# Optimization experiments

Measured on AMD Instinct MI355X. Metric: run time of the kernel, lower is better.

## Reference

```python
import jax, jax.numpy as jnp
import numpy as np

N = 50000      # total nodes
E = 400000     # edges (before self-loops)
F_IN = 75      # atom features
H = 4          # GAT heads (layers 1,2)
C = 128        # hidden_channels
G = 512        # graphs in batch
EPS_BN = 1e-5


def setup_inputs() -> dict:
    key = jax.random.key(0)
    ks = jax.random.split(key, 32)
    inp = {}
    inp["x"] = jax.random.normal(ks[0], (N, F_IN), jnp.float32)
    inp["edge_index"] = jax.random.randint(ks[1], (2, E), 0, N, dtype=jnp.int32)
    inp["batch"] = jnp.sort(jax.random.randint(ks[2], (N,), 0, G, dtype=jnp.int32))
    # (in_dim, heads, out_per_head, concat)
    dims = [(F_IN, H, C, True), (H * C, H, C, True), (H * C, 1, C, False)]
    i = 3
    for li, (din, h, c, concat) in enumerate(dims, 1):
        dout = h * c if concat else c
        s = 1.0 / np.sqrt(din)
        inp[f"W{li}"] = jax.random.normal(ks[i], (din, h * c), jnp.float32) * s
        inp[f"as{li}"] = jax.random.normal(ks[i + 1], (h, c), jnp.float32) * 0.1
        inp[f"ad{li}"] = jax.random.normal(ks[i + 2], (h, c), jnp.float32) * 0.1
        inp[f"b{li}"] = jnp.zeros((dout,), jnp.float32)
        inp[f"g{li}"] = jnp.ones((dout,), jnp.float32)
        inp[f"bt{li}"] = jnp.zeros((dout,), jnp.float32)
        inp[f"rm{li}"] = jax.random.normal(ks[i + 3], (dout,), jnp.float32) * 0.05
        inp[f"rv{li}"] = jnp.ones((dout,), jnp.float32)
        i += 4
    return inp


def gat_layer(x, src, dst, W, a_src, a_dst, b, heads, c_out, concat):
    # x: [N, Fin] -> h: [N, H, C]
    n = x.shape[0]
    h = (x @ W).reshape(n, heads, c_out)
    # per-node attention logits [N, H]
    al_s = jnp.sum(h * a_src[None], axis=-1)
    al_d = jnp.sum(h * a_dst[None], axis=-1)
    # per-edge logits + leaky relu (PyG GATConv, slope 0.2)
    e = jax.nn.leaky_relu(al_s[src] + al_d[dst], negative_slope=0.2)  # [E, H]
    # segment softmax over destination nodes
    emax = jax.ops.segment_max(e, dst, num_segments=n)
    p = jnp.exp(e - emax[dst])
    denom = jax.ops.segment_sum(p, dst, num_segments=n)
    alpha = p / (denom[dst] + 1e-16)
    # weighted message aggregation
    msg = h[src] * alpha[:, :, None]            # [E, H, C]
    out = jax.ops.segment_sum(msg, dst, num_segments=n)  # [N, H, C]
    out = out.reshape(n, heads * c_out) if concat else out.mean(axis=1)
    return out + b


def bn_eval(x, g, bt, rm, rv):
    return (x - rm) * g * jax.lax.rsqrt(rv + EPS_BN) + bt


def reference(x, edge_index, batch,
              W1, as1, ad1, b1, g1, bt1, rm1, rv1,
              W2, as2, ad2, b2, g2, bt2, rm2, rv2,
              W3, as3, ad3, b3, g3, bt3, rm3, rv3):
    n = x.shape[0]
    ar = jnp.arange(n, dtype=edge_index.dtype)
    # GATConv adds self-loops by default
    src = jnp.concatenate([edge_index[0], ar])
    dst = jnp.concatenate([edge_index[1], ar])

    h = gat_layer(x, src, dst, W1, as1, ad1, b1, H, C, True)
    h = jax.nn.relu(bn_eval(h, g1, bt1, rm1, rv1))   # dropout off (eval)
    h = gat_layer(h, src, dst, W2, as2, ad2, b2, H, C, True)
    h = jax.nn.relu(bn_eval(h, g2, bt2, rm2, rv2))
    h = gat_layer(h, src, dst, W3, as3, ad3, b3, 1, C, False)
    h = bn_eval(h, g3, bt3, rm3, rv3)

    # global mean + max pool over graphs
    ones = jnp.ones((n,), h.dtype)
    cnt = jnp.maximum(jax.ops.segment_sum(ones, batch, num_segments=G), 1.0)
    gmean = jax.ops.segment_sum(h, batch, num_segments=G) / cnt[:, None]
    gmax = jax.ops.segment_max(h, batch, num_segments=G)
    gmax = jnp.where(jnp.isfinite(gmax), gmax, 0.0)  # guard empty graphs
    return jnp.concatenate([gmean, gmax], axis=1)    # [G, 2*C]
```

## Files before the change

### kernel.cpp

```cpp
#include <hip/hip_runtime.h>

typedef unsigned short u16;
typedef unsigned int u32;
typedef __attribute__((ext_vector_type(8))) short s16x8;
typedef __attribute__((ext_vector_type(4))) float f32x4;

__device__ __forceinline__ float bf2f(u32 u) {
    return __uint_as_float(u << 16);
}
__device__ __forceinline__ u16 f2bf(float f) {
    u32 x = __float_as_uint(f);
    u32 r = (x + 0x7fffu + ((x >> 16) & 1u)) >> 16;
    return (u16)r;
}

__device__ __forceinline__ void gload16(const u16* g, u16* l) {
    __builtin_amdgcn_global_load_lds(
        (const __attribute__((address_space(1))) unsigned int*)g,
        (__attribute__((address_space(3))) unsigned int*)l,
        16, 0, 0);
}

__device__ __forceinline__ float lk60(float e) {
    e = (e > 0.f) ? e : 0.2f * e;
    return fminf(e, 60.f);
}

__global__ __launch_bounds__(256) void cvt_all_k(
    const float* __restrict__ x, const float* __restrict__ W1,
    const float* __restrict__ W2, const float* __restrict__ W3,
    u16* __restrict__ xb, u16* __restrict__ Wt1,
    u16* __restrict__ Wt2, u16* __restrict__ Wt3, int N, int Mp)
{
    const int i = blockIdx.x * 256 + threadIdx.x;
    const int n1 = Mp * 96;
    const int n2 = 512 * 96;
    const int n3 = 512 * 512;
    const int n4 = 128 * 512;
    if (i < n1) {
        const int r = i / 96, c = i - r * 96;
        xb[i] = f2bf((r < N && c < 75) ? x[(size_t)r * 75 + c] : 0.f);
    } else if (i < n1 + n2) {
        const int j = i - n1;
        const int n = j / 96, k = j - n * 96;
        Wt1[j] = f2bf(k < 75 ? W1[(size_t)k * 512 + n] : 0.f);
    } else if (i < n1 + n2 + n3) {
        const int j = i - n1 - n2;
        const int n = j >> 9, k = j & 511;
        Wt2[j] = f2bf(W2[(size_t)k * 512 + n]);
    } else if (i < n1 + n2 + n3 + n4) {
        const int j = i - n1 - n2 - n3;
        const int n = j >> 9, k = j & 511;
        Wt3[j] = f2bf(W3[(size_t)k * 128 + n]);
    }
}

__global__ __launch_bounds__(256) void mgemm_k(
    const u16* __restrict__ A, const u16* __restrict__ Bt, u16* __restrict__ C,
    const float* __restrict__ avs, const float* __restrict__ avd,
    float* __restrict__ als, float* __restrict__ ald,
    int M, int K, int Ncol, int H, int NXB)
{
    __shared__ u16 Al[2][128 * 32];
    __shared__ u16 Bl[2][128 * 32];
    const int t = threadIdx.x;
    const int lane = t & 63;
    const int wid = t >> 6;
    const int wr = wid >> 1, wc = wid & 1;
    const int rr = lane & 15, q = lane >> 4;

    const int dd = blockIdx.x;
    const int xcd = dd & 7, ii = dd >> 3;
    const int gpx = (int)(gridDim.x >> 3) / NXB;
    const int yb = xcd * gpx + ((NXB == 4) ? (ii >> 2) : ii);
    const int head = (NXB == 4) ? (ii & 3) : 0;
    const int m0 = yb * 128, n0 = head * 128;

    f32x4 acc[4][4];
#pragma unroll
    for (int m = 0; m < 4; ++m)
#pragma unroll
        for (int n = 0; n < 4; ++n) acc[m][n] = (f32x4){0.f, 0.f, 0.f, 0.f};

    auto stage = [&](int b, int k0) {
#pragma unroll
        for (int i2 = 0; i2 < 2; ++i2) {
            const int si = i2 * 256 + t;
            const int r = si >> 2, s = si & 3;
            const int g = s ^ ((r >> 1) & 3);
            gload16(A  + (size_t)(m0 + r) * K + k0 + g * 8, &Al[b][si * 8]);
            gload16(Bt + (size_t)(n0 + r) * K + k0 + g * 8, &Bl[b][si * 8]);
        }
    };

    const int nk = K >> 5;
    stage(0, 0);
    __syncthreads();
    int buf = 0;
    for (int kt = 0; kt < nk; ++kt) {
        if (kt + 1 < nk) stage(buf ^ 1, (kt + 1) << 5);
        s16x8 af[4], bfr[4];
#pragma unroll
        for (int m = 0; m < 4; ++m) {
            const int r = wr * 64 + m * 16 + rr;
            af[m] = *reinterpret_cast<const s16x8*>(&Al[buf][r * 32 + ((q ^ ((r >> 1) & 3)) << 3)]);
        }
#pragma unroll
        for (int n = 0; n < 4; ++n) {
            const int r = wc * 64 + n * 16 + rr;
            bfr[n] = *reinterpret_cast<const s16x8*>(&Bl[buf][r * 32 + ((q ^ ((r >> 1) & 3)) << 3)]);
        }
#pragma unroll
        for (int m = 0; m < 4; ++m)
#pragma unroll
            for (int n = 0; n < 4; ++n)
                acc[m][n] = __builtin_amdgcn_mfma_f32_16x16x32_bf16(af[m], bfr[n], acc[m][n], 0, 0, 0);
        __syncthreads();
        buf ^= 1;
    }

#pragma unroll
    for (int m = 0; m < 4; ++m) {
        const int row_b = m0 + wr * 64 + m * 16 + q * 4;
#pragma unroll
        for (int j = 0; j < 4; ++j) {
            const int row = row_b + j;
            if (row < M) {
#pragma unroll
                for (int n = 0; n < 4; ++n) {
                    const int col = n0 + wc * 64 + n * 16 + rr;
                    C[(size_t)row * Ncol + col] = f2bf(acc[m][n][j]);
                }
            }
        }
    }

    float asv[4], adv[4];
#pragma unroll
    for (int n = 0; n < 4; ++n) {
        const int c = wc * 64 + n * 16 + rr;
        asv[n] = avs[head * 128 + c];
        adv[n] = avd[head * 128 + c];
    }
    float* lps = (float*)&Al[0][0];
    float* lpd = lps + 256;
#pragma unroll
    for (int m = 0; m < 4; ++m)
#pragma unroll
        for (int j = 0; j < 4; ++j) {
            float ps = 0.f, pd = 0.f;
#pragma unroll
            for (int n = 0; n < 4; ++n) {
                ps += acc[m][n][j] * asv[n];
                pd += acc[m][n][j] * adv[n];
            }
#pragma unroll
            for (int off = 1; off < 16; off <<= 1) {
                ps += __shfl_xor(ps, off, 64);
                pd += __shfl_xor(pd, off, 64);
            }
            if (rr == 0) {
                const int r = wr * 64 + m * 16 + q * 4 + j;
                lps[wc * 128 + r] = ps;
                lpd[wc * 128 + r] = pd;
            }
        }
    __syncthreads();
    if (t < 128) {
        const int row = m0 + t;
        if (row < M) {
            als[(size_t)row * H + head] = lps[t] + lps[128 + t];
            ald[(size_t)row * H + head] = lpd[t] + lpd[128 + t];
        }
    }
}

__global__ void count_k(const int* __restrict__ edst, int* __restrict__ cnt, int E_, int N_)
{
    const int i = blockIdx.x * 256 + threadIdx.x;
    if (i >= E_ + N_) return;
    const int d = (i < E_) ? edst[i] : (i - E_);
    atomicAdd(&cnt[d], 1);
}

#define SCAN_B 256
__global__ void scan1_k(const int* __restrict__ cnt, int* __restrict__ part,
                        int* __restrict__ bsum, int n)
{
    __shared__ int sm[SCAN_B];
    const int idx = blockIdx.x * SCAN_B + threadIdx.x;
    int v = (idx < n) ? cnt[idx] : 0;
    sm[threadIdx.x] = v;
    __syncthreads();
    for (int off = 1; off < SCAN_B; off <<= 1) {
        int t2 = (threadIdx.x >= off) ? sm[threadIdx.x - off] : 0;
        __syncthreads();
        sm[threadIdx.x] += t2;
        __syncthreads();
    }
    if (idx < n) part[idx] = sm[threadIdx.x];
    if (threadIdx.x == SCAN_B - 1) bsum[blockIdx.x] = sm[threadIdx.x];
}

__global__ void scan2_k(int* __restrict__ bsum, int nb)
{
    __shared__ int sm[SCAN_B];
    const int t = threadIdx.x;
    int v = (t < nb) ? bsum[t] : 0;
    sm[t] = v;
    __syncthreads();
    for (int off = 1; off < SCAN_B; off <<= 1) {
        int t2 = (t >= off) ? sm[t - off] : 0;
        __syncthreads();
        sm[t] += t2;
        __syncthreads();
    }
    if (t < nb) bsum[t] = sm[t] - v;
}

__global__ void scan3_k(const int* __restrict__ part, const int* __restrict__ boff,
                        int* __restrict__ offs, int n)
{
    const int idx = blockIdx.x * SCAN_B + threadIdx.x;
    if (idx < n) offs[idx + 1] = part[idx] + boff[idx / SCAN_B];
    if (idx == 0) offs[0] = 0;
}

__global__ void scatter_k(const int* __restrict__ esrc, const int* __restrict__ edst,
                          const int* __restrict__ offs, int* __restrict__ fill,
                          int* __restrict__ csr, int E_, int N_)
{
    const int i = blockIdx.x * 256 + threadIdx.x;
    if (i >= E_ + N_) return;
    int s, d;
    if (i < E_) { s = esrc[i]; d = edst[i]; } else { s = d = i - E_; }
    const int pos = offs[d] + atomicAdd(&fill[d], 1);
    csr[pos] = s;
}

template<bool RELU>
__global__ __launch_bounds__(256) void agg512_k(
    const u16* __restrict__ hsrc, const int* __restrict__ offs,
    const int* __restrict__ csr, const float* __restrict__ als,
    const float* __restrict__ ald, const float* __restrict__ bias,
    const float* __restrict__ gam, const float* __restrict__ bet,
    const float* __restrict__ rmean, const float* __restrict__ rvar,
    u16* __restrict__ outp, int N)
{
    const int lane = threadIdx.x & 63;
    const int dst = blockIdx.x * 4 + (threadIdx.x >> 6);
    if (dst >= N) return;
    const int ch0 = lane * 8;
    const int hd = lane >> 4;

    const float advh = ald[(size_t)dst * 4 + hd];
    const int rs = offs[dst], re = offs[dst + 1];

    float acc[8] = {};
    float smw = 0.f;
    int s = rs;
    for (; s + 4 <= re; s += 4) {
        int sn[4];
#pragma unroll
        for (int u = 0; u < 4; ++u) sn[u] = csr[s + u];
        int4 r[4];
#pragma unroll
        for (int u = 0; u < 4; ++u)
            r[u] = *reinterpret_cast<const int4*>(hsrc + (size_t)sn[u] * 512 + ch0);
        float aa[4];
#pragma unroll
        for (int u = 0; u < 4; ++u)
            aa[u] = __expf(lk60(als[(size_t)sn[u] * 4 + hd] + advh));
#pragma unroll
        for (int u = 0; u < 4; ++u) {
            smw += aa[u];
            const u32 rr2[4] = {(u32)r[u].x, (u32)r[u].y, (u32)r[u].z, (u32)r[u].w};
#pragma unroll
            for (int qq = 0; qq < 4; ++qq) {
                acc[2*qq]   += aa[u] * bf2f(rr2[qq] & 0xffffu);
                acc[2*qq+1] += aa[u] * bf2f(rr2[qq] >> 16);
            }
        }
    }
    for (; s < re; ++s) {
        const int sn = csr[s];
        const float a = __expf(lk60(als[(size_t)sn * 4 + hd] + advh));
        smw += a;
        const int4 r = *reinterpret_cast<const int4*>(hsrc + (size_t)sn * 512 + ch0);
        const u32 rr2[4] = {(u32)r.x, (u32)r.y, (u32)r.z, (u32)r.w};
#pragma unroll
        for (int qq = 0; qq < 4; ++qq) {
            acc[2*qq]   += a * bf2f(rr2[qq] & 0xffffu);
            acc[2*qq+1] += a * bf2f(rr2[qq] >> 16);
        }
    }
    const float inv = 1.f / (smw + 1e-16f);

    u16 ob[8];
#pragma unroll
    for (int j = 0; j < 8; ++j) {
        const int ch = ch0 + j;
        const float scale = gam[ch] * rsqrtf(rvar[ch] + 1e-5f);
        float val = (acc[j] * inv + bias[ch] - rmean[ch]) * scale + bet[ch];
        if (RELU) val = fmaxf(val, 0.f);
        ob[j] = f2bf(val);
    }
    int4 w;
    w.x = (int)((u32)ob[0] | ((u32)ob[1] << 16));
    w.y = (int)((u32)ob[2] | ((u32)ob[3] << 16));
    w.z = (int)((u32)ob[4] | ((u32)ob[5] << 16));
    w.w = (int)((u32)ob[6] | ((u32)ob[7] << 16));
    *reinterpret_cast<int4*>(outp + (size_t)dst * 512 + ch0) = w;
}

__global__ __launch_bounds__(256) void agg128_k(
    const u16* __restrict__ hsrc, const int* __restrict__ offs,
    const int* __restrict__ csr, const float* __restrict__ als,
    const float* __restrict__ ald, const float* __restrict__ bias,
    const float* __restrict__ gam, const float* __restrict__ bet,
    const float* __restrict__ rmean, const float* __restrict__ rvar,
    u16* __restrict__ outp, int N)
{
    const int tid = threadIdx.x;
    const int w = tid >> 6, g = (tid >> 4) & 3, l = tid & 15;
    const int dst = blockIdx.x * 16 + w * 4 + g;
    if (dst >= N) return;
    const int ch0 = l * 8;

    const float advh = ald[dst];
    const int rs = offs[dst], re = offs[dst + 1];

    float acc[8] = {};
    float smw = 0.f;
    int s = rs;
    for (; s + 4 <= re; s += 4) {
        int sn[4];
#pragma unroll
        for (int u = 0; u < 4; ++u) sn[u] = csr[s + u];
        int4 r[4];
#pragma unroll
        for (int u = 0; u < 4; ++u)
            r[u] = *reinterpret_cast<const int4*>(hsrc + (size_t)sn[u] * 128 + ch0);
        float aa[4];
#pragma unroll
        for (int u = 0; u < 4; ++u)
            aa[u] = __expf(lk60(als[sn[u]] + advh));
#pragma unroll
        for (int u = 0; u < 4; ++u) {
            smw += aa[u];
            const u32 rr2[4] = {(u32)r[u].x, (u32)r[u].y, (u32)r[u].z, (u32)r[u].w};
#pragma unroll
            for (int qq = 0; qq < 4; ++qq) {
                acc[2*qq]   += aa[u] * bf2f(rr2[qq] & 0xffffu);
                acc[2*qq+1] += aa[u] * bf2f(rr2[qq] >> 16);
            }
        }
    }
    for (; s < re; ++s) {
        const int sn = csr[s];
        const float a = __expf(lk60(als[sn] + advh));
        smw += a;
        const int4 r = *reinterpret_cast<const int4*>(hsrc + (size_t)sn * 128 + ch0);
        const u32 rr2[4] = {(u32)r.x, (u32)r.y, (u32)r.z, (u32)r.w};
#pragma unroll
        for (int qq = 0; qq < 4; ++qq) {
            acc[2*qq]   += a * bf2f(rr2[qq] & 0xffffu);
            acc[2*qq+1] += a * bf2f(rr2[qq] >> 16);
        }
    }
    const float inv = 1.f / (smw + 1e-16f);

    u16 ob[8];
#pragma unroll
    for (int j = 0; j < 8; ++j) {
        const int ch = ch0 + j;
        const float scale = gam[ch] * rsqrtf(rvar[ch] + 1e-5f);
        float val = (acc[j] * inv + bias[ch] - rmean[ch]) * scale + bet[ch];
        ob[j] = f2bf(val);
    }
    int4 wv;
    wv.x = (int)((u32)ob[0] | ((u32)ob[1] << 16));
    wv.y = (int)((u32)ob[2] | ((u32)ob[3] << 16));
    wv.z = (int)((u32)ob[4] | ((u32)ob[5] << 16));
    wv.w = (int)((u32)ob[6] | ((u32)ob[7] << 16));
    *reinterpret_cast<int4*>(outp + (size_t)dst * 128 + ch0) = wv;
}

__global__ __launch_bounds__(128) void pool_k(
    const u16* __restrict__ h3, const int* __restrict__ batch,
    float* __restrict__ out, int N)
{
    const int g = blockIdx.x;
    const int t = threadIdx.x;
    int lo = 0, hi = N;
    while (lo < hi) { int mid = (lo + hi) >> 1; if (batch[mid] < g) lo = mid + 1; else hi = mid; }
    const int s0 = lo;
    lo = 0; hi = N;
    while (lo < hi) { int mid = (lo + hi) >> 1; if (batch[mid] < g + 1) lo = mid + 1; else hi = mid; }
    const int s1 = lo;
    float sum = 0.f, mx = -1e30f;
    for (int n = s0; n < s1; ++n) {
        const float v = bf2f((u32)h3[(size_t)n * 128 + t]);
        sum += v;
        mx = fmaxf(mx, v);
    }
    const int cnt = s1 - s0;
    out[(size_t)g * 256 + t]       = cnt ? sum / (float)cnt : 0.f;
    out[(size_t)g * 256 + 128 + t] = cnt ? mx : 0.f;
}

extern "C" void kernel_launch(void* const* d_in, const int* in_sizes, int n_in,
                              void* d_out, int out_size, void* d_ws, size_t ws_size,
                              hipStream_t stream)
{
    const float* x   = (const float*)d_in[0];
    const int* ei    = (const int*)d_in[1];
    const int* batch = (const int*)d_in[2];
    const float* W1  = (const float*)d_in[3];
    const float* as1 = (const float*)d_in[4];
    const float* ad1 = (const float*)d_in[5];
    const float* b1  = (const float*)d_in[6];
    const float* g1  = (const float*)d_in[7];
    const float* bt1 = (const float*)d_in[8];
    const float* rm1 = (const float*)d_in[9];
    const float* rv1 = (const float*)d_in[10];
    const float* W2  = (const float*)d_in[11];
    const float* as2 = (const float*)d_in[12];
    const float* ad2 = (const float*)d_in[13];
    const float* b2  = (const float*)d_in[14];
    const float* g2  = (const float*)d_in[15];
    const float* bt2 = (const float*)d_in[16];
    const float* rm2 = (const float*)d_in[17];
    const float* rv2 = (const float*)d_in[18];
    const float* W3  = (const float*)d_in[19];
    const float* as3 = (const float*)d_in[20];
    const float* ad3 = (const float*)d_in[21];
    const float* b3  = (const float*)d_in[22];
    const float* g3  = (const float*)d_in[23];
    const float* bt3 = (const float*)d_in[24];
    const float* rm3 = (const float*)d_in[25];
    const float* rv3 = (const float*)d_in[26];

    const int Nn = in_sizes[2];
    const int Ee = in_sizes[1] / 2;
    const int ET = Ee + Nn;
    const int Gg = out_size / 256;
    const int Mp = 392 * 128;

    char* ws = (char*)d_ws;
    size_t o = 0;
    auto alc = [&](size_t bytes) { size_t r = o; o = (o + bytes + 255) & ~(size_t)255; return r; };
    u16*  hA   = (u16*)(ws + alc((size_t)Mp * 512 * 2));
    u16*  hB   = (u16*)(ws + alc((size_t)Mp * 512 * 2));
    u16*  xb   = (u16*)(ws + alc((size_t)Mp * 96 * 2));
    u16*  Wt1  = (u16*)(ws + alc((size_t)512 * 96 * 2));
    u16*  Wt2  = (u16*)(ws + alc((size_t)512 * 512 * 2));
    u16*  Wt3  = (u16*)(ws + alc((size_t)128 * 512 * 2));
    float* als = (float*)(ws + alc((size_t)Nn * 4 * 4));
    float* ald = (float*)(ws + alc((size_t)Nn * 4 * 4));
    int*  cnt  = (int*)(ws + alc((size_t)2 * Nn * 4));
    int*  fill = cnt + Nn;
    int*  offs = (int*)(ws + alc((size_t)(Nn + 1) * 4));
    int*  part = (int*)(ws + alc((size_t)Nn * 4));
    int*  bsum = (int*)(ws + alc((size_t)SCAN_B * 4));
    int*  csr  = (int*)(ws + alc((size_t)ET * 4));
    (void)ws_size; (void)n_in;

    hipMemsetAsync(cnt, 0, (size_t)2 * Nn * 4, stream);
    const int ETB = (ET + 255) / 256;
    count_k<<<ETB, 256, 0, stream>>>(ei + Ee, cnt, Ee, Nn);
    const int nb = (Nn + SCAN_B - 1) / SCAN_B;
    scan1_k<<<nb, SCAN_B, 0, stream>>>(cnt, part, bsum, Nn);
    scan2_k<<<1, SCAN_B, 0, stream>>>(bsum, nb);
    scan3_k<<<nb, SCAN_B, 0, stream>>>(part, bsum, offs, Nn);
    scatter_k<<<ETB, 256, 0, stream>>>(ei, ei + Ee, offs, fill, csr, Ee, Nn);

    {
        const int tot = Mp * 96 + 512 * 96 + 512 * 512 + 128 * 512;
        cvt_all_k<<<(tot + 255) / 256, 256, 0, stream>>>(x, W1, W2, W3,
                                                         xb, Wt1, Wt2, Wt3, Nn, Mp);
    }

    const int nwb4  = (Nn + 3) / 4;
    const int nwb16 = (Nn + 15) / 16;
    const int nwg4 = 392 * 4;
    const int nwg1 = 392;

    mgemm_k<<<nwg4, 256, 0, stream>>>(xb, Wt1, hA, as1, ad1, als, ald, Nn, 96, 512, 4, 4);
    agg512_k<true><<<nwb4, 256, 0, stream>>>(hA, offs, csr, als, ald,
                                             b1, g1, bt1, rm1, rv1, hB, Nn);
    mgemm_k<<<nwg4, 256, 0, stream>>>(hB, Wt2, hA, as2, ad2, als, ald, Nn, 512, 512, 4, 4);
    agg512_k<true><<<nwb4, 256, 0, stream>>>(hA, offs, csr, als, ald,
                                             b2, g2, bt2, rm2, rv2, hB, Nn);
    mgemm_k<<<nwg1, 256, 0, stream>>>(hB, Wt3, hA, as3, ad3, als, ald, Nn, 512, 128, 1, 1);
    agg128_k<<<nwb16, 256, 0, stream>>>(hA, offs, csr, als, ald,
                                        b3, g3, bt3, rm3, rv3, hB, Nn);
    pool_k<<<Gg, 128, 0, stream>>>(hB, batch, (float*)d_out, Nn);
}
```

Measured before the change: 370.7 us.

## Split 512-wide aggregation into channel slices and merge prep/scan kernels

The 512-channel aggregation kernel now assigns each block one 64-channel slice (of eight) across 32 destinations, with 8 lanes per destination, instead of one wavefront per destination covering all channels. This gives more, smaller gathers and makes blocks with the same slice index share a head's feature columns, aiming at better cache locality and load balance. Separately, the degree count is fused into the conversion kernel and the three-kernel scan is replaced by a single 1024-thread block scan, cutting launch overhead. In exchange, the csr index list and attention logits are re-read once per slice, and the single-block scan is serial per thread.

```diff
diff --git a/kernel.cpp b/kernel.cpp
--- a/kernel.cpp
+++ b/kernel.cpp
@@ -26,13 +26,21 @@
     return fminf(e, 60.f);
 }
 
-__global__ __launch_bounds__(256) void cvt_all_k(
+__global__ __launch_bounds__(256) void prep_k(
+    const int* __restrict__ edst,  int* __restrict__ cnt, int E_,
     const float* __restrict__ x, const float* __restrict__ W1,
     const float* __restrict__ W2, const float* __restrict__ W3,
     u16* __restrict__ xb, u16* __restrict__ Wt1,
-    u16* __restrict__ Wt2, u16* __restrict__ Wt3, int N, int Mp)
-{
-    const int i = blockIdx.x * 256 + threadIdx.x;
+    u16* __restrict__ Wt2, u16* __restrict__ Wt3, int N, int Mp, int ETB)
+{
+    if ((int)blockIdx.x < ETB) {
+        const int i = blockIdx.x * 256 + threadIdx.x;
+        if (i >= E_ + N) return;
+        const int d = (i < E_) ? edst[i] : (i - E_);
+        atomicAdd(&cnt[d], 1);
+        return;
+    }
+    const int i = ((int)blockIdx.x - ETB) * 256 + threadIdx.x;
     const int n1 = Mp * 96;
     const int n2 = 512 * 96;
     const int n3 = 512 * 512;
@@ -55,6 +63,34 @@
     }
 }
 
+__global__ __launch_bounds__(1024) void scan_one_k(
+    const int* __restrict__ cnt, int* __restrict__ offs, int n)
+{
+    __shared__ int part[1024];
+    const int t = threadIdx.x;
+    const int per = (n + 1023) / 1024;
+    const int base = t * per;
+    int sum = 0;
+    for (int i = 0; i < per; ++i) {
+        const int idx = base + i;
+        if (idx < n) { sum += cnt[idx]; offs[idx + 1] = sum; }
+    }
+    part[t] = sum;
+    __syncthreads();
+    for (int off = 1; off < 1024; off <<= 1) {
+        int v = (t >= off) ? part[t - off] : 0;
+        __syncthreads();
+        part[t] += v;
+        __syncthreads();
+    }
+    const int excl = part[t] - sum;
+    for (int i = 0; i < per; ++i) {
+        const int idx = base + i;
+        if (idx < n) offs[idx + 1] += excl;
+    }
+    if (t == 0) offs[0] = 0;
+}
+
 __global__ __launch_bounds__(256) void mgemm_k(
     const u16* __restrict__ A, const u16* __restrict__ Bt, u16* __restrict__ C,
     const float* __restrict__ avs, const float* __restrict__ avd,
@@ -175,57 +211,6 @@
     }
 }
 
-__global__ void count_k(const int* __restrict__ edst, int* __restrict__ cnt, int E_, int N_)
-{
-    const int i = blockIdx.x * 256 + threadIdx.x;
-    if (i >= E_ + N_) return;
-    const int d = (i < E_) ? edst[i] : (i - E_);
-    atomicAdd(&cnt[d], 1);
-}
-
-#define SCAN_B 256
-__global__ void scan1_k(const int* __restrict__ cnt, int* __restrict__ part,
-                        int* __restrict__ bsum, int n)
-{
-    __shared__ int sm[SCAN_B];
-    const int idx = blockIdx.x * SCAN_B + threadIdx.x;
-    int v = (idx < n) ? cnt[idx] : 0;
-    sm[threadIdx.x] = v;
-    __syncthreads();
-    for (int off = 1; off < SCAN_B; off <<= 1) {
-        int t2 = (threadIdx.x >= off) ? sm[threadIdx.x - off] : 0;
-        __syncthreads();
-        sm[threadIdx.x] += t2;
-        __syncthreads();
-    }
-    if (idx < n) part[idx] = sm[threadIdx.x];
-    if (threadIdx.x == SCAN_B - 1) bsum[blockIdx.x] = sm[threadIdx.x];
-}
-
-__global__ void scan2_k(int* __restrict__ bsum, int nb)
-{
-    __shared__ int sm[SCAN_B];
-    const int t = threadIdx.x;
-    int v = (t < nb) ? bsum[t] : 0;
-    sm[t] = v;
-    __syncthreads();
-    for (int off = 1; off < SCAN_B; off <<= 1) {
-        int t2 = (t >= off) ? sm[t - off] : 0;
-        __syncthreads();
-        sm[t] += t2;
-        __syncthreads();
-    }
-    if (t < nb) bsum[t] = sm[t] - v;
-}
-
-__global__ void scan3_k(const int* __restrict__ part, const int* __restrict__ boff,
-                        int* __restrict__ offs, int n)
-{
-    const int idx = blockIdx.x * SCAN_B + threadIdx.x;
-    if (idx < n) offs[idx + 1] = part[idx] + boff[idx / SCAN_B];
-    if (idx == 0) offs[0] = 0;
-}
-
 __global__ void scatter_k(const int* __restrict__ esrc, const int* __restrict__ edst,
                           const int* __restrict__ offs, int* __restrict__ fill,
                           int* __restrict__ csr, int E_, int N_)
@@ -239,7 +224,7 @@
 }
 
 template<bool RELU>
-__global__ __launch_bounds__(256) void agg512_k(
+__global__ __launch_bounds__(256) void agg512s_k(
     const u16* __restrict__ hsrc, const int* __restrict__ offs,
     const int* __restrict__ csr, const float* __restrict__ als,
     const float* __restrict__ ald, const float* __restrict__ bias,
@@ -247,11 +232,16 @@
     const float* __restrict__ rmean, const float* __restrict__ rvar,
     u16* __restrict__ outp, int N)
 {
-    const int lane = threadIdx.x & 63;
-    const int dst = blockIdx.x * 4 + (threadIdx.x >> 6);
+    const int blk = blockIdx.x;
+    const int slice = blk & 7, gi = blk >> 3;
+    const int t = threadIdx.x;
+    const int w = t >> 6;
+    const int lane = t & 63;
+    const int g = lane >> 3, l = lane & 7;
+    const int dst = gi * 32 + w * 8 + g;
     if (dst >= N) return;
-    const int ch0 = lane * 8;
-    const int hd = lane >> 4;
+    const int ch0 = slice * 64 + l * 8;
+    const int hd = slice >> 1;
 
     const float advh = ald[(size_t)dst * 4 + hd];
     const int rs = offs[dst], re = offs[dst + 1];
@@ -305,12 +295,12 @@
         if (RELU) val = fmaxf(val, 0.f);
         ob[j] = f2bf(val);
     }
-    int4 w;
-    w.x = (int)((u32)ob[0] | ((u32)ob[1] << 16));
-    w.y = (int)((u32)ob[2] | ((u32)ob[3] << 16));
-    w.z = (int)((u32)ob[4] | ((u32)ob[5] << 16));
-    w.w = (int)((u32)ob[6] | ((u32)ob[7] << 16));
-    *reinterpret_cast<int4*>(outp + (size_t)dst * 512 + ch0) = w;
+    int4 wv;
+    wv.x = (int)((u32)ob[0] | ((u32)ob[1] << 16));
+    wv.y = (int)((u32)ob[2] | ((u32)ob[3] << 16));
+    wv.z = (int)((u32)ob[4] | ((u32)ob[5] << 16));
+    wv.w = (int)((u32)ob[6] | ((u32)ob[7] << 16));
+    *reinterpret_cast<int4*>(outp + (size_t)dst * 512 + ch0) = wv;
 }
 
 __global__ __launch_bounds__(256) void agg128_k(
@@ -461,37 +451,33 @@
     int*  cnt  = (int*)(ws + alc((size_t)2 * Nn * 4));
     int*  fill = cnt + Nn;
     int*  offs = (int*)(ws + alc((size_t)(Nn + 1) * 4));
-    int*  part = (int*)(ws + alc((size_t)Nn * 4));
-    int*  bsum = (int*)(ws + alc((size_t)SCAN_B * 4));
     int*  csr  = (int*)(ws + alc((size_t)ET * 4));
     (void)ws_size; (void)n_in;
 
+    const int ETB = (ET + 255) / 256;
+
     hipMemsetAsync(cnt, 0, (size_t)2 * Nn * 4, stream);
-    const int ETB = (ET + 255) / 256;
-    count_k<<<ETB, 256, 0, stream>>>(ei + Ee, cnt, Ee, Nn);
-    const int nb = (Nn + SCAN_B - 1) / SCAN_B;
-    scan1_k<<<nb, SCAN_B, 0, stream>>>(cnt, part, bsum, Nn);
-    scan2_k<<<1, SCAN_B, 0, stream>>>(bsum, nb);
-    scan3_k<<<nb, SCAN_B, 0, stream>>>(part, bsum, offs, Nn);
+    {
+        const int cvt_tot = Mp * 96 + 512 * 96 + 512 * 512 + 128 * 512;
+        const int cvtB = (cvt_tot + 255) / 256;
+        prep_k<<<ETB + cvtB, 256, 0, stream>>>(ei + Ee, cnt, Ee,
+                                               x, W1, W2, W3,
+                                               xb, Wt1, Wt2, Wt3, Nn, Mp, ETB);
+    }
+    scan_one_k<<<1, 1024, 0, stream>>>(cnt, offs, Nn);
     scatter_k<<<ETB, 256, 0, stream>>>(ei, ei + Ee, offs, fill, csr, Ee, Nn);
 
-    {
-        const int tot = Mp * 96 + 512 * 96 + 512 * 512 + 128 * 512;
-        cvt_all_k<<<(tot + 255) / 256, 256, 0, stream>>>(x, W1, W2, W3,
-                                                         xb, Wt1, Wt2, Wt3, Nn, Mp);
-    }
-
-    const int nwb4  = (Nn + 3) / 4;
+    const int nbs32 = (Nn + 31) / 32;
     const int nwb16 = (Nn + 15) / 16;
     const int nwg4 = 392 * 4;
     const int nwg1 = 392;
 
     mgemm_k<<<nwg4, 256, 0, stream>>>(xb, Wt1, hA, as1, ad1, als, ald, Nn, 96, 512, 4, 4);
-    agg512_k<true><<<nwb4, 256, 0, stream>>>(hA, offs, csr, als, ald,
-                                             b1, g1, bt1, rm1, rv1, hB, Nn);
+    agg512s_k<true><<<8 * nbs32, 256, 0, stream>>>(hA, offs, csr, als, ald,
+                                                   b1, g1, bt1, rm1, rv1, hB, Nn);
     mgemm_k<<<nwg4, 256, 0, stream>>>(hB, Wt2, hA, as2, ad2, als, ald, Nn, 512, 512, 4, 4);
-    agg512_k<true><<<nwb4, 256, 0, stream>>>(hA, offs, csr, als, ald,
-                                             b2, g2, bt2, rm2, rv2, hB, Nn);
+    agg512s_k<true><<<8 * nbs32, 256, 0, stream>>>(hA, offs, csr, als, ald,
+                                                   b2, g2, bt2, rm2, rv2, hB, Nn);
     mgemm_k<<<nwg1, 256, 0, stream>>>(hB, Wt3, hA, as3, ad3, als, ald, Nn, 512, 128, 1, 1);
     agg128_k<<<nwb16, 256, 0, stream>>>(hA, offs, csr, als, ald,
                                         b3, g3, bt3, rm3, rv3, hB, Nn);
```

New measurement: 509.1 us. 1.37x slower.

## Slice 512-channel aggregation across blocks by channel group and fuse count with conversion

Applied to the files above, without the earlier changes.

The 512-channel GAT aggregation kernel is remapped so that each block handles one 64-channel slice for 32 destination nodes, with 8 lanes per node, instead of one wavefront covering all 512 channels of a node. The slice index sits in the low bits of the block id, so neighbouring blocks touch the same rows of the source features, which is meant to improve cache locality on the gathers and balance irregular degrees. The in-degree counting kernel is also merged into the weight/input conversion kernel to save a launch. In exchange, CSR offsets, attention logits and edge indices are reread once per slice, eight times in total.

```diff
diff --git a/kernel.cpp b/kernel.cpp
--- a/kernel.cpp
+++ b/kernel.cpp
@@ -26,13 +26,21 @@
     return fminf(e, 60.f);
 }
 
-__global__ __launch_bounds__(256) void cvt_all_k(
+__global__ __launch_bounds__(256) void prep_k(
+    const int* __restrict__ edst,  int* __restrict__ cnt, int E_,
     const float* __restrict__ x, const float* __restrict__ W1,
     const float* __restrict__ W2, const float* __restrict__ W3,
     u16* __restrict__ xb, u16* __restrict__ Wt1,
-    u16* __restrict__ Wt2, u16* __restrict__ Wt3, int N, int Mp)
-{
-    const int i = blockIdx.x * 256 + threadIdx.x;
+    u16* __restrict__ Wt2, u16* __restrict__ Wt3, int N, int Mp, int ETB)
+{
+    if ((int)blockIdx.x < ETB) {
+        const int i = blockIdx.x * 256 + threadIdx.x;
+        if (i >= E_ + N) return;
+        const int d = (i < E_) ? edst[i] : (i - E_);
+        atomicAdd(&cnt[d], 1);
+        return;
+    }
+    const int i = ((int)blockIdx.x - ETB) * 256 + threadIdx.x;
     const int n1 = Mp * 96;
     const int n2 = 512 * 96;
     const int n3 = 512 * 512;
@@ -55,134 +63,6 @@
     }
 }
 
-__global__ __launch_bounds__(256) void mgemm_k(
-    const u16* __restrict__ A, const u16* __restrict__ Bt, u16* __restrict__ C,
-    const float* __restrict__ avs, const float* __restrict__ avd,
-    float* __restrict__ als, float* __restrict__ ald,
-    int M, int K, int Ncol, int H, int NXB)
-{
-    __shared__ u16 Al[2][128 * 32];
-    __shared__ u16 Bl[2][128 * 32];
-    const int t = threadIdx.x;
-    const int lane = t & 63;
-    const int wid = t >> 6;
-    const int wr = wid >> 1, wc = wid & 1;
-    const int rr = lane & 15, q = lane >> 4;
-
-    const int dd = blockIdx.x;
-    const int xcd = dd & 7, ii = dd >> 3;
-    const int gpx = (int)(gridDim.x >> 3) / NXB;
-    const int yb = xcd * gpx + ((NXB == 4) ? (ii >> 2) : ii);
-    const int head = (NXB == 4) ? (ii & 3) : 0;
-    const int m0 = yb * 128, n0 = head * 128;
-
-    f32x4 acc[4][4];
-#pragma unroll
-    for (int m = 0; m < 4; ++m)
-#pragma unroll
-        for (int n = 0; n < 4; ++n) acc[m][n] = (f32x4){0.f, 0.f, 0.f, 0.f};
-
-    auto stage = [&](int b, int k0) {
-#pragma unroll
-        for (int i2 = 0; i2 < 2; ++i2) {
-            const int si = i2 * 256 + t;
-            const int r = si >> 2, s = si & 3;
-            const int g = s ^ ((r >> 1) & 3);
-            gload16(A  + (size_t)(m0 + r) * K + k0 + g * 8, &Al[b][si * 8]);
-            gload16(Bt + (size_t)(n0 + r) * K + k0 + g * 8, &Bl[b][si * 8]);
-        }
-    };
-
-    const int nk = K >> 5;
-    stage(0, 0);
-    __syncthreads();
-    int buf = 0;
-    for (int kt = 0; kt < nk; ++kt) {
-        if (kt + 1 < nk) stage(buf ^ 1, (kt + 1) << 5);
-        s16x8 af[4], bfr[4];
-#pragma unroll
-        for (int m = 0; m < 4; ++m) {
-            const int r = wr * 64 + m * 16 + rr;
-            af[m] = *reinterpret_cast<const s16x8*>(&Al[buf][r * 32 + ((q ^ ((r >> 1) & 3)) << 3)]);
-        }
-#pragma unroll
-        for (int n = 0; n < 4; ++n) {
-            const int r = wc * 64 + n * 16 + rr;
-            bfr[n] = *reinterpret_cast<const s16x8*>(&Bl[buf][r * 32 + ((q ^ ((r >> 1) & 3)) << 3)]);
-        }
-#pragma unroll
-        for (int m = 0; m < 4; ++m)
-#pragma unroll
-            for (int n = 0; n < 4; ++n)
-                acc[m][n] = __builtin_amdgcn_mfma_f32_16x16x32_bf16(af[m], bfr[n], acc[m][n], 0, 0, 0);
-        __syncthreads();
-        buf ^= 1;
-    }
-
-#pragma unroll
-    for (int m = 0; m < 4; ++m) {
-        const int row_b = m0 + wr * 64 + m * 16 + q * 4;
-#pragma unroll
-        for (int j = 0; j < 4; ++j) {
-            const int row = row_b + j;
-            if (row < M) {
-#pragma unroll
-                for (int n = 0; n < 4; ++n) {
-                    const int col = n0 + wc * 64 + n * 16 + rr;
-                    C[(size_t)row * Ncol + col] = f2bf(acc[m][n][j]);
-                }
-            }
-        }
-    }
-
-    float asv[4], adv[4];
-#pragma unroll
-    for (int n = 0; n < 4; ++n) {
-        const int c = wc * 64 + n * 16 + rr;
-        asv[n] = avs[head * 128 + c];
-        adv[n] = avd[head * 128 + c];
-    }
-    float* lps = (float*)&Al[0][0];
-    float* lpd = lps + 256;
-#pragma unroll
-    for (int m = 0; m < 4; ++m)
-#pragma unroll
-        for (int j = 0; j < 4; ++j) {
-            float ps = 0.f, pd = 0.f;
-#pragma unroll
-            for (int n = 0; n < 4; ++n) {
-                ps += acc[m][n][j] * asv[n];
-                pd += acc[m][n][j] * adv[n];
-            }
-#pragma unroll
-            for (int off = 1; off < 16; off <<= 1) {
-                ps += __shfl_xor(ps, off, 64);
-                pd += __shfl_xor(pd, off, 64);
-            }
-            if (rr == 0) {
-                const int r = wr * 64 + m * 16 + q * 4 + j;
-                lps[wc * 128 + r] = ps;
-                lpd[wc * 128 + r] = pd;
-            }
-        }
-    __syncthreads();
-    if (t < 128) {
-        const int row = m0 + t;
-        if (row < M) {
-            als[(size_t)row * H + head] = lps[t] + lps[128 + t];
-            ald[(size_t)row * H + head] = lpd[t] + lpd[128 + t];
-        }
-    }
-}
-
-__global__ void count_k(const int* __restrict__ edst, int* __restrict__ cnt, int E_, int N_)
-{
-    const int i = blockIdx.x * 256 + threadIdx.x;
-    if (i >= E_ + N_) return;
-    const int d = (i < E_) ? edst[i] : (i - E_);
-    atomicAdd(&cnt[d], 1);
-}
-
 #define SCAN_B 256
 __global__ void scan1_k(const int* __restrict__ cnt, int* __restrict__ part,
                         int* __restrict__ bsum, int n)
@@ -226,6 +106,126 @@
     if (idx == 0) offs[0] = 0;
 }
 
+__global__ __launch_bounds__(256) void mgemm_k(
+    const u16* __restrict__ A, const u16* __restrict__ Bt, u16* __restrict__ C,
+    const float* __restrict__ avs, const float* __restrict__ avd,
+    float* __restrict__ als, float* __restrict__ ald,
+    int M, int K, int Ncol, int H, int NXB)
+{
+    __shared__ u16 Al[2][128 * 32];
+    __shared__ u16 Bl[2][128 * 32];
+    const int t = threadIdx.x;
+    const int lane = t & 63;
+    const int wid = t >> 6;
+    const int wr = wid >> 1, wc = wid & 1;
+    const int rr = lane & 15, q = lane >> 4;
+
+    const int dd = blockIdx.x;
+    const int xcd = dd & 7, ii = dd >> 3;
+    const int gpx = (int)(gridDim.x >> 3) / NXB;
+    const int yb = xcd * gpx + ((NXB == 4) ? (ii >> 2) : ii);
+    const int head = (NXB == 4) ? (ii & 3) : 0;
+    const int m0 = yb * 128, n0 = head * 128;
+
+    f32x4 acc[4][4];
+#pragma unroll
+    for (int m = 0; m < 4; ++m)
+#pragma unroll
+        for (int n = 0; n < 4; ++n) acc[m][n] = (f32x4){0.f, 0.f, 0.f, 0.f};
+
+    auto stage = [&](int b, int k0) {
+#pragma unroll
+        for (int i2 = 0; i2 < 2; ++i2) {
+            const int si = i2 * 256 + t;
+            const int r = si >> 2, s = si & 3;
+            const int g = s ^ ((r >> 1) & 3);
+            gload16(A  + (size_t)(m0 + r) * K + k0 + g * 8, &Al[b][si * 8]);
+            gload16(Bt + (size_t)(n0 + r) * K + k0 + g * 8, &Bl[b][si * 8]);
+        }
+    };
+
+    const int nk = K >> 5;
+    stage(0, 0);
+    __syncthreads();
+    int buf = 0;
+    for (int kt = 0; kt < nk; ++kt) {
+        if (kt + 1 < nk) stage(buf ^ 1, (kt + 1) << 5);
+        s16x8 af[4], bfr[4];
+#pragma unroll
+        for (int m = 0; m < 4; ++m) {
+            const int r = wr * 64 + m * 16 + rr;
+            af[m] = *reinterpret_cast<const s16x8*>(&Al[buf][r * 32 + ((q ^ ((r >> 1) & 3)) << 3)]);
+        }
+#pragma unroll
+        for (int n = 0; n < 4; ++n) {
+            const int r = wc * 64 + n * 16 + rr;
+            bfr[n] = *reinterpret_cast<const s16x8*>(&Bl[buf][r * 32 + ((q ^ ((r >> 1) & 3)) << 3)]);
+        }
+#pragma unroll
+        for (int m = 0; m < 4; ++m)
+#pragma unroll
+            for (int n = 0; n < 4; ++n)
+                acc[m][n] = __builtin_amdgcn_mfma_f32_16x16x32_bf16(af[m], bfr[n], acc[m][n], 0, 0, 0);
+        __syncthreads();
+        buf ^= 1;
+    }
+
+#pragma unroll
+    for (int m = 0; m < 4; ++m) {
+        const int row_b = m0 + wr * 64 + m * 16 + q * 4;
+#pragma unroll
+        for (int j = 0; j < 4; ++j) {
+            const int row = row_b + j;
+            if (row < M) {
+#pragma unroll
+                for (int n = 0; n < 4; ++n) {
+                    const int col = n0 + wc * 64 + n * 16 + rr;
+                    C[(size_t)row * Ncol + col] = f2bf(acc[m][n][j]);
+                }
+            }
+        }
+    }
+
+    float asv[4], adv[4];
+#pragma unroll
+    for (int n = 0; n < 4; ++n) {
+        const int c = wc * 64 + n * 16 + rr;
+        asv[n] = avs[head * 128 + c];
+        adv[n] = avd[head * 128 + c];
+    }
+    float* lps = (float*)&Al[0][0];
+    float* lpd = lps + 256;
+#pragma unroll
+    for (int m = 0; m < 4; ++m)
+#pragma unroll
+        for (int j = 0; j < 4; ++j) {
+            float ps = 0.f, pd = 0.f;
+#pragma unroll
+            for (int n = 0; n < 4; ++n) {
+                ps += acc[m][n][j] * asv[n];
+                pd += acc[m][n][j] * adv[n];
+            }
+#pragma unroll
+            for (int off = 1; off < 16; off <<= 1) {
+                ps += __shfl_xor(ps, off, 64);
+                pd += __shfl_xor(pd, off, 64);
+            }
+            if (rr == 0) {
+                const int r = wr * 64 + m * 16 + q * 4 + j;
+                lps[wc * 128 + r] = ps;
+                lpd[wc * 128 + r] = pd;
+            }
+        }
+    __syncthreads();
+    if (t < 128) {
+        const int row = m0 + t;
+        if (row < M) {
+            als[(size_t)row * H + head] = lps[t] + lps[128 + t];
+            ald[(size_t)row * H + head] = lpd[t] + lpd[128 + t];
+        }
+    }
+}
+
 __global__ void scatter_k(const int* __restrict__ esrc, const int* __restrict__ edst,
                           const int* __restrict__ offs, int* __restrict__ fill,
                           int* __restrict__ csr, int E_, int N_)
@@ -239,7 +239,7 @@
 }
 
 template<bool RELU>
-__global__ __launch_bounds__(256) void agg512_k(
+__global__ __launch_bounds__(256) void agg512s_k(
     const u16* __restrict__ hsrc, const int* __restrict__ offs,
     const int* __restrict__ csr, const float* __restrict__ als,
     const float* __restrict__ ald, const float* __restrict__ bias,
@@ -247,11 +247,16 @@
     const float* __restrict__ rmean, const float* __restrict__ rvar,
     u16* __restrict__ outp, int N)
 {
-    const int lane = threadIdx.x & 63;
-    const int dst = blockIdx.x * 4 + (threadIdx.x >> 6);
+    const int blk = blockIdx.x;
+    const int slice = blk & 7, gi = blk >> 3;
+    const int t = threadIdx.x;
+    const int w = t >> 6;
+    const int lane = t & 63;
+    const int g = lane >> 3, l = lane & 7;
+    const int dst = gi * 32 + w * 8 + g;
     if (dst >= N) return;
-    const int ch0 = lane * 8;
-    const int hd = lane >> 4;
+    const int ch0 = slice * 64 + l * 8;
+    const int hd = slice >> 1;
 
     const float advh = ald[(size_t)dst * 4 + hd];
     const int rs = offs[dst], re = offs[dst + 1];
@@ -305,12 +310,12 @@
         if (RELU) val = fmaxf(val, 0.f);
         ob[j] = f2bf(val);
     }
-    int4 w;
-    w.x = (int)((u32)ob[0] | ((u32)ob[1] << 16));
-    w.y = (int)((u32)ob[2] | ((u32)ob[3] << 16));
-    w.z = (int)((u32)ob[4] | ((u32)ob[5] << 16));
-    w.w = (int)((u32)ob[6] | ((u32)ob[7] << 16));
-    *reinterpret_cast<int4*>(outp + (size_t)dst * 512 + ch0) = w;
+    int4 wv;
+    wv.x = (int)((u32)ob[0] | ((u32)ob[1] << 16));
+    wv.y = (int)((u32)ob[2] | ((u32)ob[3] << 16));
+    wv.z = (int)((u32)ob[4] | ((u32)ob[5] << 16));
+    wv.w = (int)((u32)ob[6] | ((u32)ob[7] << 16));
+    *reinterpret_cast<int4*>(outp + (size_t)dst * 512 + ch0) = wv;
 }
 
 __global__ __launch_bounds__(256) void agg128_k(
@@ -466,32 +471,33 @@
     int*  csr  = (int*)(ws + alc((size_t)ET * 4));
     (void)ws_size; (void)n_in;
 
+    const int ETB = (ET + 255) / 256;
+
     hipMemsetAsync(cnt, 0, (size_t)2 * Nn * 4, stream);
-    const int ETB = (ET + 255) / 256;
-    count_k<<<ETB, 256, 0, stream>>>(ei + Ee, cnt, Ee, Nn);
+    {
+        const int cvt_tot = Mp * 96 + 512 * 96 + 512 * 512 + 128 * 512;
+        const int cvtB = (cvt_tot + 255) / 256;
+        prep_k<<<ETB + cvtB, 256, 0, stream>>>(ei + Ee, cnt, Ee,
+                                               x, W1, W2, W3,
+                                               xb, Wt1, Wt2, Wt3, Nn, Mp, ETB);
+    }
     const int nb = (Nn + SCAN_B - 1) / SCAN_B;
     scan1_k<<<nb, SCAN_B, 0, stream>>>(cnt, part, bsum, Nn);
     scan2_k<<<1, SCAN_B, 0, stream>>>(bsum, nb);
     scan3_k<<<nb, SCAN_B, 0, stream>>>(part, bsum, offs, Nn);
     scatter_k<<<ETB, 256, 0, stream>>>(ei, ei + Ee, offs, fill, csr, Ee, Nn);
 
-    {
-        const int tot = Mp * 96 + 512 * 96 + 512 * 512 + 128 * 512;
-        cvt_all_k<<<(tot + 255) / 256, 256, 0, stream>>>(x, W1, W2, W3,
-                                                         xb, Wt1, Wt2, Wt3, Nn, Mp);
-    }
-
-    const int nwb4  = (Nn + 3) / 4;
+    const int nbs32 = (Nn + 31) / 32;
     const int nwb16 = (Nn + 15) / 16;
     const int nwg4 = 392 * 4;
     const int nwg1 = 392;
 
     mgemm_k<<<nwg4, 256, 0, stream>>>(xb, Wt1, hA, as1, ad1, als, ald, Nn, 96, 512, 4, 4);
-    agg512_k<true><<<nwb4, 256, 0, stream>>>(hA, offs, csr, als, ald,
-                                             b1, g1, bt1, rm1, rv1, hB, Nn);
+    agg512s_k<true><<<8 * nbs32, 256, 0, stream>>>(hA, offs, csr, als, ald,
+                                                   b1, g1, bt1, rm1, rv1, hB, Nn);
     mgemm_k<<<nwg4, 256, 0, stream>>>(hB, Wt2, hA, as2, ad2, als, ald, Nn, 512, 512, 4, 4);
-    agg512_k<true><<<nwb4, 256, 0, stream>>>(hA, offs, csr, als, ald,
-                                             b2, g2, bt2, rm2, rv2, hB, Nn);
+    agg512s_k<true><<<8 * nbs32, 256, 0, stream>>>(hA, offs, csr, als, ald,
+                                                   b2, g2, bt2, rm2, rv2, hB, Nn);
     mgemm_k<<<nwg1, 256, 0, stream>>>(hB, Wt3, hA, as3, ad3, als, ald, Nn, 512, 128, 1, 1);
     agg128_k<<<nwb16, 256, 0, stream>>>(hA, offs, csr, als, ald,
                                         b3, g3, bt3, rm3, rv3, hB, Nn);
```

New measurement: 366.3 us. Within noise of the previous version (-1.2%).
